# Optimization experiments

Measured on AMD Instinct MI355X. Metric: run time of the kernel, lower is better.

The kernel has to match this reference:

```python
import jax, jax.numpy as jnp
import numpy as np

# DCRNN (PEMS-BAY scale) constants
N = 325      # num_nodes
B = 64       # batch_size
T = 12       # encoder seq_len
HZ = 12      # decoder horizon
U = 64       # rnn_units
DIN = 2      # input_dim
DOUT = 1     # output_dim
K = 2        # max_diffusion_step
NM = K + 1   # num diffusion matrices (Chebyshev, single laplacian support)


def _glorot(key, shape):
    lim = float(np.sqrt(6.0 / (shape[0] + shape[1])))
    return jax.random.uniform(key, shape, jnp.float32, -lim, lim)


def setup_inputs() -> dict:
    key = jax.random.key(0)
    ks = jax.random.split(key, 8)
    # random symmetric adjacency -> scaled Laplacian support (lambda_max ~= 2 approx)
    a = np.asarray(jax.random.uniform(ks[0], (N, N)))
    a = (a + a.T) * 0.5
    a = a * (a > 0.9)
    d = a.sum(1)
    dinv = 1.0 / np.sqrt(np.maximum(d, 1e-8))
    L = np.eye(N, dtype=np.float32) - (dinv[:, None] * a * dinv[None, :]).astype(np.float32)
    support = jnp.asarray(L - np.eye(N, dtype=np.float32))  # 2L/lambda_max - I with lambda_max=2

    def cell_params(k, din):
        f = (din + U) * NM
        k1, k2 = jax.random.split(k)
        return dict(gate_W=_glorot(k1, (f, 2 * U)), gate_b=jnp.zeros((2 * U,), jnp.float32),
                    cand_W=_glorot(k2, (f, U)), cand_b=jnp.zeros((U,), jnp.float32))

    inp = {"inputs": jax.random.normal(ks[1], (T, B, N * DIN), jnp.float32),
           "support": support}
    for name, din, kk in [("enc0", DIN, ks[2]), ("enc1", U, ks[3]),
                          ("dec0", DOUT, ks[4]), ("dec1", U, ks[5])]:
        for pn, v in cell_params(kk, din).items():
            inp[f"{name}_{pn}"] = v
    inp["proj_W"] = _glorot(ks[6], (U, DOUT))
    inp["proj_b"] = jnp.zeros((DOUT,), jnp.float32)
    return inp


def _gconv(x, support, W, b):
    # x: (B, N, F). Chebyshev diffusion: x0=x, x1=Lx, x2=2Lx1-x0, ...
    xs = [x]
    x0, x1 = x, jnp.einsum('mn,bnf->bmf', support, x)
    xs.append(x1)
    for _ in range(2, K + 1):
        x2 = 2.0 * jnp.einsum('mn,bnf->bmf', support, x1) - x0
        xs.append(x2)
        x0, x1 = x1, x2
    xk = jnp.concatenate(xs, axis=-1)  # (B, N, NM*F)
    return xk @ W + b


def _gru_cell(x, h, support, gW, gb, cW, cb):
    # diffusion-conv GRU: r,u gates then candidate
    ru = jax.nn.sigmoid(_gconv(jnp.concatenate([x, h], -1), support, gW, gb))
    r, u = jnp.split(ru, 2, axis=-1)
    c = jnp.tanh(_gconv(jnp.concatenate([x, r * h], -1), support, cW, cb))
    return u * h + (1.0 - u) * c


def reference(inputs, support,
              enc0_gate_W, enc0_gate_b, enc0_cand_W, enc0_cand_b,
              enc1_gate_W, enc1_gate_b, enc1_cand_W, enc1_cand_b,
              dec0_gate_W, dec0_gate_b, dec0_cand_W, dec0_cand_b,
              dec1_gate_W, dec1_gate_b, dec1_cand_W, dec1_cand_b,
              proj_W, proj_b):
    x_seq = inputs.reshape(T, B, N, DIN)
    h0 = jnp.zeros((B, N, U), inputs.dtype)

    def enc_step(carry, x):
        h_l0, h_l1 = carry
        h_l0 = _gru_cell(x, h_l0, support, enc0_gate_W, enc0_gate_b, enc0_cand_W, enc0_cand_b)
        h_l1 = _gru_cell(h_l0, h_l1, support, enc1_gate_W, enc1_gate_b, enc1_cand_W, enc1_cand_b)
        return (h_l0, h_l1), None

    (h_l0, h_l1), _ = jax.lax.scan(enc_step, (h0, h0), x_seq)

    def dec_step(carry, _):
        d_in, hd0, hd1 = carry
        hd0 = _gru_cell(d_in, hd0, support, dec0_gate_W, dec0_gate_b, dec0_cand_W, dec0_cand_b)
        hd1 = _gru_cell(hd0, hd1, support, dec1_gate_W, dec1_gate_b, dec1_cand_W, dec1_cand_b)
        out = hd1 @ proj_W + proj_b  # (B, N, DOUT)
        return (out, hd0, hd1), out.reshape(B, N * DOUT)

    start = jnp.zeros((B, N, DOUT), inputs.dtype)  # GO symbol
    _, outputs = jax.lax.scan(dec_step, (start, h_l0, h_l1), None, length=HZ)
    return outputs  # (horizon, B, N*DOUT)
```

## Files before the change

kernel.cpp:

```cpp
#include <hip/hip_runtime.h>

constexpr int N  = 325;
constexpr int B  = 64;
constexpr int T  = 12;
constexpr int HZ = 12;
constexpr int U  = 64;
constexpr int BN = B * N;

constexpr int SSM   = 672;
constexpr int SSTIL = 42;
constexpr int SSKC  = 11;

typedef __attribute__((ext_vector_type(8))) short short8;
typedef __attribute__((ext_vector_type(4))) float floatx4;

__device__ inline unsigned short f2bf(float f) {
    unsigned u = __float_as_uint(f);
    u += 0x7fff + ((u >> 16) & 1);
    return (unsigned short)(u >> 16);
}
__device__ inline unsigned pack_hilo(float v) {
    const unsigned short hi = f2bf(v);
    const float hif = __uint_as_float(((unsigned)hi) << 16);
    const unsigned short lo = f2bf(v - hif);
    return (unsigned)hi | ((unsigned)lo << 16);
}


__global__ void zero_kernel(unsigned* __restrict__ p, long n) {
    long i = (long)blockIdx.x * blockDim.x + threadIdx.x;
    const long stride = (long)gridDim.x * blockDim.x;
    for (; i < n; i += stride) p[i] = 0u;
}

__global__ __launch_bounds__(256)
void s2_build(const float* __restrict__ S, float* __restrict__ S2)
{
    const int m = blockIdx.x;
    __shared__ float srow[N];
    for (int i = threadIdx.x; i < N; i += 256) srow[i] = S[m * N + i];
    __syncthreads();
    for (int c = threadIdx.x; c < N; c += 256) {
        float a = 0.f;
        for (int k = 0; k < N; ++k) a += srow[k] * S[k * N + c];
        S2[m * N + c] = a;
    }
}

__global__ __launch_bounds__(64)
void prepack_ss(const float* __restrict__ S, const float* __restrict__ S2,
                short* __restrict__ ssh, short* __restrict__ ssl)
{
    const int t = blockIdx.x, kc = blockIdx.y, lane = threadIdx.x;
    const int quad = lane >> 4, l15 = lane & 15;
    short8 hv, lv;
    #pragma unroll
    for (int j = 0; j < 8; ++j) {
        const int m = t * 16 + l15;
        const int k = kc * 32 + quad * 8 + j;
        float v = 0.f;
        if (k < N) {
            if (m < N) v = S[m * N + k];
            else if (m >= 336 && m < 336 + N) v = S2[(m - 336) * N + k];
        }
        const unsigned short hb = f2bf(v);
        hv[j] = (short)hb;
        lv[j] = (short)f2bf(v - __uint_as_float(((unsigned)hb) << 16));
    }
    const size_t off = ((size_t)(t * SSKC + kc) * 64 + lane);
    ((short8*)ssh)[off] = hv;
    ((short8*)ssl)[off] = lv;
}

__global__ __launch_bounds__(64)
void prepack_w(const float* __restrict__ W, short* __restrict__ Wh,
               short* __restrict__ Wl, int F, int Nout, int NT)
{
    const int kc = blockIdx.x, n = blockIdx.y, lane = threadIdx.x;
    const int quad = lane >> 4, l15 = lane & 15;
    short8 hv, lv;
    #pragma unroll
    for (int j = 0; j < 8; ++j) {
        const int k   = kc * 32 + quad * 8 + j;
        const int col = n * 16 + l15;
        const int lvl = k / F, f = k - lvl * F;
        float w = 0.f;
        if (lvl == 0)
            w = W[(size_t)f * Nout + col] - W[(size_t)(2 * F + f) * Nout + col];
        else if (lvl == 1)
            w = W[(size_t)(F + f) * Nout + col];
        else if (lvl == 2)
            w = 2.f * W[(size_t)(2 * F + f) * Nout + col];
        const unsigned short hb = f2bf(w);
        hv[j] = (short)hb;
        lv[j] = (short)f2bf(w - __uint_as_float(((unsigned)hb) << 16));
    }
    const size_t off = ((size_t)(kc * NT + n) * 64 + lane);
    ((short8*)Wh)[off] = hv;
    ((short8*)Wl)[off] = lv;
}

template<int DIN, int F, int K3P, bool RMUL>
__global__ __launch_bounds__(448, 3)
void diffuse_mfma(const short8* __restrict__ ssh, const short8* __restrict__ ssl,
                  const float* __restrict__ x, const float* __restrict__ h,
                  const float* __restrict__ ru, unsigned* __restrict__ zcat)
{
    constexpr int XST = 364;
    const int cx = blockIdx.x, b = blockIdx.y, mh = blockIdx.z;
    const int c0 = cx * 32;
    const int tid = threadIdx.x, wave = tid >> 6, lane = tid & 63;
    const int quad = lane >> 4, l15 = lane & 15;

    __shared__ unsigned xls[32 * XST];

    for (int idx = tid; idx < 352 * 32; idx += 448) {
        const int n = idx >> 5, f = idx & 31, gf = c0 + f;
        unsigned u = 0u;
        if (n < N && gf < F) {
            const int row = b * N + n;
            float v;
            if (gf < DIN) {
                v = x[(size_t)row * DIN + gf];
            } else {
                v = h[(size_t)row * U + (gf - DIN)];
                if (RMUL) v *= ru[(size_t)row * 128 + (gf - DIN)];
            }
            u = pack_hilo(v);
            if (mh == 0 && !(RMUL && gf < DIN))
                zcat[(size_t)row * K3P + gf] = u;
        }
        xls[f * XST + n] = u;
    }
    __syncthreads();

    const int tb = mh * 21 + wave * 3;

    floatx4 acc[3][2];
    #pragma unroll
    for (int i = 0; i < 3; ++i)
        #pragma unroll
        for (int n = 0; n < 2; ++n)
            acc[i][n] = (floatx4){0.f, 0.f, 0.f, 0.f};

    short8 cah[3], cal[3], nah[3], nal[3];
    #pragma unroll
    for (int i = 0; i < 3; ++i) {
        const size_t fo = (size_t)((tb + i) * SSKC) * 64 + lane;
        cah[i] = ssh[fo]; cal[i] = ssl[fo];
    }
    for (int kc = 0; kc < SSKC; ++kc) {
        if (kc + 1 < SSKC) {
            #pragma unroll
            for (int i = 0; i < 3; ++i) {
                const size_t fo = (size_t)((tb + i) * SSKC + kc + 1) * 64 + lane;
                nah[i] = ssh[fo]; nal[i] = ssl[fo];
            }
        }
        short8 bh[2], bl[2];
        const int koff = kc * 32 + quad * 8;
        #pragma unroll
        for (int n = 0; n < 2; ++n) {
            const uint4 u0 = *(const uint4*)&xls[(n * 16 + l15) * XST + koff];
            const uint4 u1 = *(const uint4*)&xls[(n * 16 + l15) * XST + koff + 4];
            const unsigned uu[8] = {u0.x, u0.y, u0.z, u0.w, u1.x, u1.y, u1.z, u1.w};
            #pragma unroll
            for (int j = 0; j < 8; ++j) {
                bh[n][j] = (short)(uu[j] & 0xffffu);
                bl[n][j] = (short)(uu[j] >> 16);
            }
        }
        #pragma unroll
        for (int i = 0; i < 3; ++i)
            #pragma unroll
            for (int n = 0; n < 2; ++n) {
                acc[i][n] = __builtin_amdgcn_mfma_f32_16x16x32_bf16(cah[i], bh[n], acc[i][n], 0, 0, 0);
                acc[i][n] = __builtin_amdgcn_mfma_f32_16x16x32_bf16(cah[i], bl[n], acc[i][n], 0, 0, 0);
                acc[i][n] = __builtin_amdgcn_mfma_f32_16x16x32_bf16(cal[i], bh[n], acc[i][n], 0, 0, 0);
            }
        if (kc + 1 < SSKC) {
            #pragma unroll
            for (int i = 0; i < 3; ++i) { cah[i] = nah[i]; cal[i] = nal[i]; }
        }
    }

    #pragma unroll
    for (int i = 0; i < 3; ++i) {
        const int t = tb + i;
        #pragma unroll
        for (int n = 0; n < 2; ++n) {
            const int col = c0 + n * 16 + l15;
            if (col >= F) continue;
            #pragma unroll
            for (int r = 0; r < 4; ++r) {
                const int m = t * 16 + quad * 4 + r;
                if (m < N)
                    zcat[(size_t)(b * N + m) * K3P + F + col] = pack_hilo(acc[i][n][r]);
                else if (m >= 336 && m < 336 + N)
                    zcat[(size_t)(b * N + (m - 336)) * K3P + 2 * F + col] = pack_hilo(acc[i][n][r]);
            }
        }
    }
}

__global__ __launch_bounds__(256)
void dense_gate_mfma(const unsigned* __restrict__ zcat, int K3p,
                     const short8* __restrict__ Wh, const short8* __restrict__ Wl,
                     const float* __restrict__ bias, float* __restrict__ ru)
{
    constexpr int NT = 4;
    const int tid = threadIdx.x, wave = tid >> 6, lane = tid & 63;
    const int quad = lane >> 4, l15 = lane & 15;
    const int row0 = blockIdx.x * 64 + wave * 16;
    const int nb = blockIdx.y * NT;

    floatx4 acc[NT];
    #pragma unroll
    for (int n = 0; n < NT; ++n) {
        const float bv = bias[(nb + n) * 16 + l15];
        acc[n] = (floatx4){bv, bv, bv, bv};
    }
    const unsigned* __restrict__ zrow = zcat + (size_t)(row0 + l15) * K3p + quad * 8;
    const int KC = K3p >> 5;
    for (int kc = 0; kc < KC; ++kc) {
        const uint4* p = (const uint4*)(zrow + kc * 32);
        const uint4 u0 = p[0], u1 = p[1];
        const unsigned uu[8] = {u0.x, u0.y, u0.z, u0.w, u1.x, u1.y, u1.z, u1.w};
        short8 ahi, alo;
        #pragma unroll
        for (int j = 0; j < 8; ++j) {
            ahi[j] = (short)(uu[j] & 0xffffu);
            alo[j] = (short)(uu[j] >> 16);
        }
        const short8* __restrict__ wh = Wh + (size_t)(kc * 8 + nb) * 64 + lane;
        const short8* __restrict__ wl = Wl + (size_t)(kc * 8 + nb) * 64 + lane;
        #pragma unroll
        for (int n = 0; n < NT; ++n) {
            const short8 bh = wh[n * 64], bl = wl[n * 64];
            acc[n] = __builtin_amdgcn_mfma_f32_16x16x32_bf16(ahi, bh, acc[n], 0, 0, 0);
            acc[n] = __builtin_amdgcn_mfma_f32_16x16x32_bf16(ahi, bl, acc[n], 0, 0, 0);
            acc[n] = __builtin_amdgcn_mfma_f32_16x16x32_bf16(alo, bh, acc[n], 0, 0, 0);
        }
    }
    #pragma unroll
    for (int n = 0; n < NT; ++n) {
        const int col = (nb + n) * 16 + l15;
        #pragma unroll
        for (int r = 0; r < 4; ++r) {
            const int row = row0 + quad * 4 + r;
            ru[(size_t)row * 128 + col] = 1.f / (1.f + __expf(-acc[n][r]));
        }
    }
}

template<bool PROJ>
__global__ __launch_bounds__(256)
void dense_cand_mfma(const unsigned* __restrict__ zcat, int K3p,
                     const short8* __restrict__ Wh, const short8* __restrict__ Wl,
                     const float* __restrict__ bias, const float* __restrict__ ru,
                     float* __restrict__ h, const float* __restrict__ pW,
                     const float* __restrict__ pb, float* __restrict__ outp,
                     float* __restrict__ dec_in)
{
    constexpr int NT = PROJ ? 4 : 2;
    const int tid = threadIdx.x, wave = tid >> 6, lane = tid & 63;
    const int quad = lane >> 4, l15 = lane & 15;
    const int row0 = blockIdx.x * 64 + wave * 16;
    const int nb = PROJ ? 0 : blockIdx.y * NT;

    floatx4 acc[NT];
    #pragma unroll
    for (int n = 0; n < NT; ++n) {
        const float bv = bias[(nb + n) * 16 + l15];
        acc[n] = (floatx4){bv, bv, bv, bv};
    }
    const unsigned* __restrict__ zrow = zcat + (size_t)(row0 + l15) * K3p + quad * 8;
    const int KC = K3p >> 5;
    for (int kc = 0; kc < KC; ++kc) {
        const uint4* p = (const uint4*)(zrow + kc * 32);
        const uint4 u0 = p[0], u1 = p[1];
        const unsigned uu[8] = {u0.x, u0.y, u0.z, u0.w, u1.x, u1.y, u1.z, u1.w};
        short8 ahi, alo;
        #pragma unroll
        for (int j = 0; j < 8; ++j) {
            ahi[j] = (short)(uu[j] & 0xffffu);
            alo[j] = (short)(uu[j] >> 16);
        }
        const short8* __restrict__ wh = Wh + (size_t)(kc * 4 + nb) * 64 + lane;
        const short8* __restrict__ wl = Wl + (size_t)(kc * 4 + nb) * 64 + lane;
        #pragma unroll
        for (int n = 0; n < NT; ++n) {
            const short8 bh = wh[n * 64], bl = wl[n * 64];
            acc[n] = __builtin_amdgcn_mfma_f32_16x16x32_bf16(ahi, bh, acc[n], 0, 0, 0);
            acc[n] = __builtin_amdgcn_mfma_f32_16x16x32_bf16(ahi, bl, acc[n], 0, 0, 0);
            acc[n] = __builtin_amdgcn_mfma_f32_16x16x32_bf16(alo, bh, acc[n], 0, 0, 0);
        }
    }
    float pr[4] = {0.f, 0.f, 0.f, 0.f};
    #pragma unroll
    for (int n = 0; n < NT; ++n) {
        const int col = (nb + n) * 16 + l15;
        float pw = 0.f;
        if constexpr (PROJ) pw = pW[col];
        #pragma unroll
        for (int r = 0; r < 4; ++r) {
            const int row = row0 + quad * 4 + r;
            const float c  = tanhf(acc[n][r]);
            const float ug = ru[(size_t)row * 128 + 64 + col];
            const float hv = h[(size_t)row * 64 + col];
            const float hn = ug * hv + (1.f - ug) * c;
            h[(size_t)row * 64 + col] = hn;
            if constexpr (PROJ) pr[r] += hn * pw;
        }
    }
    if constexpr (PROJ) {
        #pragma unroll
        for (int r = 0; r < 4; ++r) {
            float v = pr[r];
            v += __shfl_xor(v, 1); v += __shfl_xor(v, 2);
            v += __shfl_xor(v, 4); v += __shfl_xor(v, 8);
            if (l15 == 0) {
                const int row = row0 + quad * 4 + r;
                const float o = v + pb[0];
                outp[row]   = o;
                dec_in[row] = o;
            }
        }
    }
}


extern "C" void kernel_launch(void* const* d_in, const int* in_sizes, int n_in,
                              void* d_out, int out_size, void* d_ws, size_t ws_size,
                              hipStream_t stream)
{
    const float* inputs = (const float*)d_in[0];
    const float* S      = (const float*)d_in[1];
    const float* Wt[4][4];
    for (int l = 0; l < 4; ++l)
        for (int j = 0; j < 4; ++j)
            Wt[l][j] = (const float*)d_in[2 + l * 4 + j];
    const float* pW = (const float*)d_in[18];
    const float* pb = (const float*)d_in[19];
    float* out = (float*)d_out;

    float*    ws     = (float*)d_ws;
    float*    h0     = ws;
    float*    h1     = h0 + (size_t)BN * U;
    float*    dec_in = h1 + (size_t)BN * U;
    float*    ru     = dec_in + BN;
    unsigned* zcat   = (unsigned*)(ru + (size_t)BN * 128);
    float*    S2     = (float*)(zcat + (size_t)BN * 384);
    char*     pp     = (char*)(S2 + (size_t)N * N);
    pp = (char*)(((uintptr_t)pp + 15) & ~(uintptr_t)15);

    short* ssh = (short*)pp;
    short* ssl = ssh + (size_t)SSTIL * SSKC * 64 * 8;
    char*  wpbase = (char*)(ssl + (size_t)SSTIL * SSKC * 64 * 8);

    const int Fs[4]   = {66, 128, 65, 128};
    const int K3ps[4] = {224, 384, 224, 384};
    short *Wgh[4], *Wgl[4], *Wch[4], *Wcl[4];
    size_t off = 0;
    for (int l = 0; l < 4; ++l) {
        const size_t ge = (size_t)K3ps[l] * 128, ce = (size_t)K3ps[l] * 64;
        Wgh[l] = (short*)(wpbase + off); off += ge * 2;
        Wgl[l] = (short*)(wpbase + off); off += ge * 2;
        Wch[l] = (short*)(wpbase + off); off += ce * 2;
        Wcl[l] = (short*)(wpbase + off); off += ce * 2;
    }

    const long zn = (long)BN * (U + U + 128) + BN + (long)BN * 384;
    zero_kernel<<<2048, 256, 0, stream>>>((unsigned*)h0, zn);

    s2_build<<<N, 256, 0, stream>>>(S, S2);
    prepack_ss<<<dim3(SSTIL, SSKC), 64, 0, stream>>>(S, S2, ssh, ssl);
    for (int l = 0; l < 4; ++l) {
        prepack_w<<<dim3(K3ps[l] / 32, 8), 64, 0, stream>>>(Wt[l][0], Wgh[l], Wgl[l],
                                                            Fs[l], 128, 8);
        prepack_w<<<dim3(K3ps[l] / 32, 4), 64, 0, stream>>>(Wt[l][2], Wch[l], Wcl[l],
                                                            Fs[l], 64, 4);
    }

    const short8* SSH = (const short8*)ssh;
    const short8* SSL = (const short8*)ssl;

    for (int t = 0; t < T; ++t) {
        const float* x = inputs + (size_t)t * BN * 2;
        diffuse_mfma<2, 66, 224, false><<<dim3(3, B, 2), 448, 0, stream>>>(SSH, SSL, x, h0, ru, zcat);
        dense_gate_mfma<<<dim3(BN / 64, 2), 256, 0, stream>>>(zcat, 224, (short8*)Wgh[0], (short8*)Wgl[0], Wt[0][1], ru);
        diffuse_mfma<2, 66, 224, true><<<dim3(3, B, 2), 448, 0, stream>>>(SSH, SSL, x, h0, ru, zcat);
        dense_cand_mfma<false><<<dim3(BN / 64, 2), 256, 0, stream>>>(zcat, 224, (short8*)Wch[0], (short8*)Wcl[0],
                                                                     Wt[0][3], ru, h0, nullptr, nullptr, nullptr, nullptr);
        diffuse_mfma<64, 128, 384, false><<<dim3(4, B, 2), 448, 0, stream>>>(SSH, SSL, h0, h1, ru, zcat);
        dense_gate_mfma<<<dim3(BN / 64, 2), 256, 0, stream>>>(zcat, 384, (short8*)Wgh[1], (short8*)Wgl[1], Wt[1][1], ru);
        diffuse_mfma<64, 128, 384, true><<<dim3(4, B, 2), 448, 0, stream>>>(SSH, SSL, h0, h1, ru, zcat);
        dense_cand_mfma<false><<<dim3(BN / 64, 2), 256, 0, stream>>>(zcat, 384, (short8*)Wch[1], (short8*)Wcl[1],
                                                                     Wt[1][3], ru, h1, nullptr, nullptr, nullptr, nullptr);
    }
    for (int hz = 0; hz < HZ; ++hz) {
        diffuse_mfma<1, 65, 224, false><<<dim3(3, B, 2), 448, 0, stream>>>(SSH, SSL, dec_in, h0, ru, zcat);
        dense_gate_mfma<<<dim3(BN / 64, 2), 256, 0, stream>>>(zcat, 224, (short8*)Wgh[2], (short8*)Wgl[2], Wt[2][1], ru);
        diffuse_mfma<1, 65, 224, true><<<dim3(3, B, 2), 448, 0, stream>>>(SSH, SSL, dec_in, h0, ru, zcat);
        dense_cand_mfma<false><<<dim3(BN / 64, 2), 256, 0, stream>>>(zcat, 224, (short8*)Wch[2], (short8*)Wcl[2],
                                                                     Wt[2][3], ru, h0, nullptr, nullptr, nullptr, nullptr);
        diffuse_mfma<64, 128, 384, false><<<dim3(4, B, 2), 448, 0, stream>>>(SSH, SSL, h0, h1, ru, zcat);
        dense_gate_mfma<<<dim3(BN / 64, 2), 256, 0, stream>>>(zcat, 384, (short8*)Wgh[3], (short8*)Wgl[3], Wt[3][1], ru);
        diffuse_mfma<64, 128, 384, true><<<dim3(4, B, 2), 448, 0, stream>>>(SSH, SSL, h0, h1, ru, zcat);
        dense_cand_mfma<true><<<BN / 64, 256, 0, stream>>>(zcat, 384, (short8*)Wch[3], (short8*)Wcl[3],
                                                           Wt[3][3], ru, h1, pW, pb,
                                                           out + (size_t)hz * BN, dec_in);
    }
}
```

Before: 4.518 ms.

## Pipeline encoder layers across timesteps and skip redundant input diffusion

The encoder is skewed so that layer 0 at step s and layer 1 at step s-1 run in the same launches. Merged diffuse, gate and candidate kernels pick a layer from blockIdx.z, and each layer gets its own ru and zcat buffers. This halves the number of encoder kernel launches and puts more blocks in each grid to fill the GPU. Separately, the reset-multiplied diffusion pass for the 64-wide input layers now starts at column block 2, so the input-feature columns computed in the first pass are not diffused again. The cost is a larger workspace and extra branching inside the merged kernels.

```diff
diff --git a/kernel.cpp b/kernel.cpp
--- a/kernel.cpp
+++ b/kernel.cpp
@@ -7,9 +7,9 @@
 constexpr int U  = 64;
 constexpr int BN = B * N;
 
-constexpr int SSM   = 672;
 constexpr int SSTIL = 42;
 constexpr int SSKC  = 11;
+constexpr int XST   = 364;
 
 typedef __attribute__((ext_vector_type(8))) short short8;
 typedef __attribute__((ext_vector_type(4))) float floatx4;
@@ -24,6 +24,15 @@
     const float hif = __uint_as_float(((unsigned)hi) << 16);
     const unsigned short lo = f2bf(v - hif);
     return (unsigned)hi | ((unsigned)lo << 16);
+}
+__device__ inline void unpack8(const uint4 u0, const uint4 u1,
+                               short8& h, short8& l) {
+    const unsigned uu[8] = {u0.x, u0.y, u0.z, u0.w, u1.x, u1.y, u1.z, u1.w};
+    #pragma unroll
+    for (int j = 0; j < 8; ++j) {
+        h[j] = (short)(uu[j] & 0xffffu);
+        l[j] = (short)(uu[j] >> 16);
+    }
 }
 
 
@@ -101,18 +110,15 @@
 }
 
 template<int DIN, int F, int K3P, bool RMUL>
-__global__ __launch_bounds__(448, 3)
-void diffuse_mfma(const short8* __restrict__ ssh, const short8* __restrict__ ssl,
-                  const float* __restrict__ x, const float* __restrict__ h,
-                  const float* __restrict__ ru, unsigned* __restrict__ zcat)
-{
-    constexpr int XST = 364;
-    const int cx = blockIdx.x, b = blockIdx.y, mh = blockIdx.z;
+__device__ __forceinline__ void diffuse_body(
+    const short8* __restrict__ ssh, const short8* __restrict__ ssl,
+    const float* __restrict__ x, const float* __restrict__ h,
+    const float* __restrict__ ru, unsigned* __restrict__ zcat,
+    int cx, int b, int mh, unsigned* __restrict__ xls)
+{
     const int c0 = cx * 32;
     const int tid = threadIdx.x, wave = tid >> 6, lane = tid & 63;
     const int quad = lane >> 4, l15 = lane & 15;
-
-    __shared__ unsigned xls[32 * XST];
 
     for (int idx = tid; idx < 352 * 32; idx += 448) {
         const int n = idx >> 5, f = idx & 31, gf = c0 + f;
@@ -163,12 +169,7 @@
         for (int n = 0; n < 2; ++n) {
             const uint4 u0 = *(const uint4*)&xls[(n * 16 + l15) * XST + koff];
             const uint4 u1 = *(const uint4*)&xls[(n * 16 + l15) * XST + koff + 4];
-            const unsigned uu[8] = {u0.x, u0.y, u0.z, u0.w, u1.x, u1.y, u1.z, u1.w};
-            #pragma unroll
-            for (int j = 0; j < 8; ++j) {
-                bh[n][j] = (short)(uu[j] & 0xffffu);
-                bl[n][j] = (short)(uu[j] >> 16);
-            }
+            unpack8(u0, u1, bh[n], bl[n]);
         }
         #pragma unroll
         for (int i = 0; i < 3; ++i)
@@ -203,16 +204,15 @@
     }
 }
 
-__global__ __launch_bounds__(256)
-void dense_gate_mfma(const unsigned* __restrict__ zcat, int K3p,
-                     const short8* __restrict__ Wh, const short8* __restrict__ Wl,
-                     const float* __restrict__ bias, float* __restrict__ ru)
+
+__device__ __forceinline__ void gate_body(const unsigned* __restrict__ zcat,
+    int K3p, const short8* __restrict__ Wh, const short8* __restrict__ Wl,
+    const float* __restrict__ bias, float* __restrict__ ru, int bx, int nb)
 {
     constexpr int NT = 4;
     const int tid = threadIdx.x, wave = tid >> 6, lane = tid & 63;
     const int quad = lane >> 4, l15 = lane & 15;
-    const int row0 = blockIdx.x * 64 + wave * 16;
-    const int nb = blockIdx.y * NT;
+    const int row0 = bx * 64 + wave * 16;
 
     floatx4 acc[NT];
     #pragma unroll
@@ -224,14 +224,8 @@
     const int KC = K3p >> 5;
     for (int kc = 0; kc < KC; ++kc) {
         const uint4* p = (const uint4*)(zrow + kc * 32);
-        const uint4 u0 = p[0], u1 = p[1];
-        const unsigned uu[8] = {u0.x, u0.y, u0.z, u0.w, u1.x, u1.y, u1.z, u1.w};
         short8 ahi, alo;
-        #pragma unroll
-        for (int j = 0; j < 8; ++j) {
-            ahi[j] = (short)(uu[j] & 0xffffu);
-            alo[j] = (short)(uu[j] >> 16);
-        }
+        unpack8(p[0], p[1], ahi, alo);
         const short8* __restrict__ wh = Wh + (size_t)(kc * 8 + nb) * 64 + lane;
         const short8* __restrict__ wl = Wl + (size_t)(kc * 8 + nb) * 64 + lane;
         #pragma unroll
@@ -253,20 +247,15 @@
     }
 }
 
-template<bool PROJ>
-__global__ __launch_bounds__(256)
-void dense_cand_mfma(const unsigned* __restrict__ zcat, int K3p,
-                     const short8* __restrict__ Wh, const short8* __restrict__ Wl,
-                     const float* __restrict__ bias, const float* __restrict__ ru,
-                     float* __restrict__ h, const float* __restrict__ pW,
-                     const float* __restrict__ pb, float* __restrict__ outp,
-                     float* __restrict__ dec_in)
-{
-    constexpr int NT = PROJ ? 4 : 2;
+__device__ __forceinline__ void cand_body(const unsigned* __restrict__ zcat,
+    int K3p, const short8* __restrict__ Wh, const short8* __restrict__ Wl,
+    const float* __restrict__ bias, const float* __restrict__ ru,
+    float* __restrict__ h, int bx, int nb)
+{
+    constexpr int NT = 2;
     const int tid = threadIdx.x, wave = tid >> 6, lane = tid & 63;
     const int quad = lane >> 4, l15 = lane & 15;
-    const int row0 = blockIdx.x * 64 + wave * 16;
-    const int nb = PROJ ? 0 : blockIdx.y * NT;
+    const int row0 = bx * 64 + wave * 16;
 
     floatx4 acc[NT];
     #pragma unroll
@@ -278,14 +267,8 @@
     const int KC = K3p >> 5;
     for (int kc = 0; kc < KC; ++kc) {
         const uint4* p = (const uint4*)(zrow + kc * 32);
-        const uint4 u0 = p[0], u1 = p[1];
-        const unsigned uu[8] = {u0.x, u0.y, u0.z, u0.w, u1.x, u1.y, u1.z, u1.w};
         short8 ahi, alo;
-        #pragma unroll
-        for (int j = 0; j < 8; ++j) {
-            ahi[j] = (short)(uu[j] & 0xffffu);
-            alo[j] = (short)(uu[j] >> 16);
-        }
+        unpack8(p[0], p[1], ahi, alo);
         const short8* __restrict__ wh = Wh + (size_t)(kc * 4 + nb) * 64 + lane;
         const short8* __restrict__ wl = Wl + (size_t)(kc * 4 + nb) * 64 + lane;
         #pragma unroll
@@ -296,12 +279,89 @@
             acc[n] = __builtin_amdgcn_mfma_f32_16x16x32_bf16(alo, bh, acc[n], 0, 0, 0);
         }
     }
-    float pr[4] = {0.f, 0.f, 0.f, 0.f};
     #pragma unroll
     for (int n = 0; n < NT; ++n) {
         const int col = (nb + n) * 16 + l15;
-        float pw = 0.f;
-        if constexpr (PROJ) pw = pW[col];
+        #pragma unroll
+        for (int r = 0; r < 4; ++r) {
+            const int row = row0 + quad * 4 + r;
+            const float c  = tanhf(acc[n][r]);
+            const float ug = ru[(size_t)row * 128 + 64 + col];
+            const float hv = h[(size_t)row * 64 + col];
+            h[(size_t)row * 64 + col] = ug * hv + (1.f - ug) * c;
+        }
+    }
+}
+
+
+template<int DIN, int F, int K3P, bool RMUL, int CB>
+__global__ __launch_bounds__(448, 3)
+void diffuse_solo(const short8* __restrict__ ssh, const short8* __restrict__ ssl,
+                  const float* __restrict__ x, const float* __restrict__ h,
+                  const float* __restrict__ ru, unsigned* __restrict__ zcat)
+{
+    __shared__ __align__(16) unsigned xls[32 * XST];
+    diffuse_body<DIN, F, K3P, RMUL>(ssh, ssl, x, h, ru, zcat,
+                                    CB + blockIdx.x, blockIdx.y, blockIdx.z, xls);
+}
+
+__global__ __launch_bounds__(256)
+void gate_solo(const unsigned* __restrict__ zcat, int K3p,
+               const short8* __restrict__ Wh, const short8* __restrict__ Wl,
+               const float* __restrict__ bias, float* __restrict__ ru)
+{
+    gate_body(zcat, K3p, Wh, Wl, bias, ru, blockIdx.x, blockIdx.y * 4);
+}
+
+__global__ __launch_bounds__(256)
+void cand_solo(const unsigned* __restrict__ zcat, int K3p,
+               const short8* __restrict__ Wh, const short8* __restrict__ Wl,
+               const float* __restrict__ bias, const float* __restrict__ ru,
+               float* __restrict__ h)
+{
+    cand_body(zcat, K3p, Wh, Wl, bias, ru, h, blockIdx.x, blockIdx.y * 2);
+}
+
+__global__ __launch_bounds__(256)
+void cand_proj(const unsigned* __restrict__ zcat, int K3p,
+               const short8* __restrict__ Wh, const short8* __restrict__ Wl,
+               const float* __restrict__ bias, const float* __restrict__ ru,
+               float* __restrict__ h, const float* __restrict__ pW,
+               const float* __restrict__ pb, float* __restrict__ outp,
+               float* __restrict__ dec_in)
+{
+    constexpr int NT = 4;
+    const int tid = threadIdx.x, wave = tid >> 6, lane = tid & 63;
+    const int quad = lane >> 4, l15 = lane & 15;
+    const int row0 = blockIdx.x * 64 + wave * 16;
+
+    floatx4 acc[NT];
+    #pragma unroll
+    for (int n = 0; n < NT; ++n) {
+        const float bv = bias[n * 16 + l15];
+        acc[n] = (floatx4){bv, bv, bv, bv};
+    }
+    const unsigned* __restrict__ zrow = zcat + (size_t)(row0 + l15) * K3p + quad * 8;
+    const int KC = K3p >> 5;
+    for (int kc = 0; kc < KC; ++kc) {
+        const uint4* p = (const uint4*)(zrow + kc * 32);
+        short8 ahi, alo;
+        unpack8(p[0], p[1], ahi, alo);
+        const short8* __restrict__ wh = Wh + (size_t)(kc * 4) * 64 + lane;
+        const short8* __restrict__ wl = Wl + (size_t)(kc * 4) * 64 + lane;
+        #pragma unroll
+        for (int n = 0; n < NT; ++n) {
+            const short8 bh = wh[n * 64], bl = wl[n * 64];
+            acc[n] = __builtin_amdgcn_mfma_f32_16x16x32_bf16(ahi, bh, acc[n], 0, 0, 0);
+            acc[n] = __builtin_amdgcn_mfma_f32_16x16x32_bf16(ahi, bl, acc[n], 0, 0, 0);
+            acc[n] = __builtin_amdgcn_mfma_f32_16x16x32_bf16(alo, bh, acc[n], 0, 0, 0);
+        }
+    }
+    float pr[4] = {0.f, 0.f, 0.f, 0.f};
+    #pragma unroll
+    for (int n = 0; n < NT; ++n) {
+        const int col = n * 16 + l15;
+        const float pw = pW[col];
         #pragma unroll
         for (int r = 0; r < 4; ++r) {
             const int row = row0 + quad * 4 + r;
@@ -310,23 +370,76 @@
             const float hv = h[(size_t)row * 64 + col];
             const float hn = ug * hv + (1.f - ug) * c;
             h[(size_t)row * 64 + col] = hn;
-            if constexpr (PROJ) pr[r] += hn * pw;
-        }
-    }
-    if constexpr (PROJ) {
-        #pragma unroll
-        for (int r = 0; r < 4; ++r) {
-            float v = pr[r];
-            v += __shfl_xor(v, 1); v += __shfl_xor(v, 2);
-            v += __shfl_xor(v, 4); v += __shfl_xor(v, 8);
-            if (l15 == 0) {
-                const int row = row0 + quad * 4 + r;
-                const float o = v + pb[0];
-                outp[row]   = o;
-                dec_in[row] = o;
-            }
-        }
-    }
+            pr[r] += hn * pw;
+        }
+    }
+    #pragma unroll
+    for (int r = 0; r < 4; ++r) {
+        float v = pr[r];
+        v += __shfl_xor(v, 1); v += __shfl_xor(v, 2);
+        v += __shfl_xor(v, 4); v += __shfl_xor(v, 8);
+        if (l15 == 0) {
+            const int row = row0 + quad * 4 + r;
+            const float o = v + pb[0];
+            outp[row]   = o;
+            dec_in[row] = o;
+        }
+    }
+}
+
+
+struct DuoDP {
+    const short8 *ssh, *ssl;
+    const float *xA, *hA, *ruA; unsigned* zA;
+    const float *xB, *hB, *ruB; unsigned* zB;
+    int cbB;
+};
+
+template<bool RM>
+__global__ __launch_bounds__(448, 3)
+void diffuse_duo(DuoDP P)
+{
+    __shared__ __align__(16) unsigned xls[32 * XST];
+    const int zz = blockIdx.z;
+    if (zz < 2) {
+        if ((int)blockIdx.x < 3)
+            diffuse_body<2, 66, 224, RM>(P.ssh, P.ssl, P.xA, P.hA, P.ruA, P.zA,
+                                         blockIdx.x, blockIdx.y, zz, xls);
+    } else {
+        if ((int)blockIdx.x < 4 - P.cbB)
+            diffuse_body<64, 128, 384, RM>(P.ssh, P.ssl, P.xB, P.hB, P.ruB, P.zB,
+                                           P.cbB + blockIdx.x, blockIdx.y, zz - 2, xls);
+    }
+}
+
+struct DuoGP {
+    const unsigned* zA; const short8 *WhA, *WlA; const float* bA; float* ruA;
+    const unsigned* zB; const short8 *WhB, *WlB; const float* bB; float* ruB;
+};
+
+__global__ __launch_bounds__(256)
+void gate_duo(DuoGP P)
+{
+    if (blockIdx.z == 0)
+        gate_body(P.zA, 224, P.WhA, P.WlA, P.bA, P.ruA, blockIdx.x, blockIdx.y * 4);
+    else
+        gate_body(P.zB, 384, P.WhB, P.WlB, P.bB, P.ruB, blockIdx.x, blockIdx.y * 4);
+}
+
+struct DuoCP {
+    const unsigned* zA; const short8 *WhA, *WlA; const float* bA;
+    const float* ruA; float* hA;
+    const unsigned* zB; const short8 *WhB, *WlB; const float* bB;
+    const float* ruB; float* hB;
+};
+
+__global__ __launch_bounds__(256)
+void cand_duo(DuoCP P)
+{
+    if (blockIdx.z == 0)
+        cand_body(P.zA, 224, P.WhA, P.WlA, P.bA, P.ruA, P.hA, blockIdx.x, blockIdx.y * 2);
+    else
+        cand_body(P.zB, 384, P.WhB, P.WlB, P.bB, P.ruB, P.hB, blockIdx.x, blockIdx.y * 2);
 }
 
 
@@ -348,9 +461,11 @@
     float*    h0     = ws;
     float*    h1     = h0 + (size_t)BN * U;
     float*    dec_in = h1 + (size_t)BN * U;
-    float*    ru     = dec_in + BN;
-    unsigned* zcat   = (unsigned*)(ru + (size_t)BN * 128);
-    float*    S2     = (float*)(zcat + (size_t)BN * 384);
+    float*    ruA    = dec_in + BN;
+    float*    ruB    = ruA + (size_t)BN * 128;
+    unsigned* zcatA  = (unsigned*)(ruB + (size_t)BN * 128);
+    unsigned* zcatB  = zcatA + (size_t)BN * 224;
+    float*    S2     = (float*)(zcatB + (size_t)BN * 384);
     char*     pp     = (char*)(S2 + (size_t)N * N);
     pp = (char*)(((uintptr_t)pp + 15) & ~(uintptr_t)15);
 
@@ -370,7 +485,7 @@
         Wcl[l] = (short*)(wpbase + off); off += ce * 2;
     }
 
-    const long zn = (long)BN * (U + U + 128) + BN + (long)BN * 384;
+    const long zn = (long)BN * (2 * U) + BN + (long)BN * 256 + (long)BN * (224 + 384);
     zero_kernel<<<2048, 256, 0, stream>>>((unsigned*)h0, zn);
 
     s2_build<<<N, 256, 0, stream>>>(S, S2);
@@ -385,30 +500,58 @@
     const short8* SSH = (const short8*)ssh;
     const short8* SSL = (const short8*)ssl;
 
-    for (int t = 0; t < T; ++t) {
-        const float* x = inputs + (size_t)t * BN * 2;
-        diffuse_mfma<2, 66, 224, false><<<dim3(3, B, 2), 448, 0, stream>>>(SSH, SSL, x, h0, ru, zcat);
-        dense_gate_mfma<<<dim3(BN / 64, 2), 256, 0, stream>>>(zcat, 224, (short8*)Wgh[0], (short8*)Wgl[0], Wt[0][1], ru);
-        diffuse_mfma<2, 66, 224, true><<<dim3(3, B, 2), 448, 0, stream>>>(SSH, SSL, x, h0, ru, zcat);
-        dense_cand_mfma<false><<<dim3(BN / 64, 2), 256, 0, stream>>>(zcat, 224, (short8*)Wch[0], (short8*)Wcl[0],
-                                                                     Wt[0][3], ru, h0, nullptr, nullptr, nullptr, nullptr);
-        diffuse_mfma<64, 128, 384, false><<<dim3(4, B, 2), 448, 0, stream>>>(SSH, SSL, h0, h1, ru, zcat);
-        dense_gate_mfma<<<dim3(BN / 64, 2), 256, 0, stream>>>(zcat, 384, (short8*)Wgh[1], (short8*)Wgl[1], Wt[1][1], ru);
-        diffuse_mfma<64, 128, 384, true><<<dim3(4, B, 2), 448, 0, stream>>>(SSH, SSL, h0, h1, ru, zcat);
-        dense_cand_mfma<false><<<dim3(BN / 64, 2), 256, 0, stream>>>(zcat, 384, (short8*)Wch[1], (short8*)Wcl[1],
-                                                                     Wt[1][3], ru, h1, nullptr, nullptr, nullptr, nullptr);
-    }
+    for (int s = 0; s <= T; ++s) {
+        const float* x0 = inputs + (size_t)s * BN * 2;
+        const bool a = (s < T), b1 = (s >= 1);
+        if (a && b1) {
+            DuoDP dp{SSH, SSL, x0, h0, nullptr, zcatA, h0, h1, nullptr, zcatB, 0};
+            diffuse_duo<false><<<dim3(4, B, 4), 448, 0, stream>>>(dp);
+            DuoGP gp{zcatA, (short8*)Wgh[0], (short8*)Wgl[0], Wt[0][1], ruA,
+                     zcatB, (short8*)Wgh[1], (short8*)Wgl[1], Wt[1][1], ruB};
+            gate_duo<<<dim3(BN / 64, 2, 2), 256, 0, stream>>>(gp);
+            DuoDP dp2{SSH, SSL, x0, h0, ruA, zcatA, h0, h1, ruB, zcatB, 2};
+            diffuse_duo<true><<<dim3(3, B, 4), 448, 0, stream>>>(dp2);
+            DuoCP cp{zcatA, (short8*)Wch[0], (short8*)Wcl[0], Wt[0][3], ruA, h0,
+                     zcatB, (short8*)Wch[1], (short8*)Wcl[1], Wt[1][3], ruB, h1};
+            cand_duo<<<dim3(BN / 64, 2, 2), 256, 0, stream>>>(cp);
+        } else if (a) {
+            diffuse_solo<2, 66, 224, false, 0><<<dim3(3, B, 2), 448, 0, stream>>>(
+                SSH, SSL, x0, h0, nullptr, zcatA);
+            gate_solo<<<dim3(BN / 64, 2), 256, 0, stream>>>(
+                zcatA, 224, (short8*)Wgh[0], (short8*)Wgl[0], Wt[0][1], ruA);
+            diffuse_solo<2, 66, 224, true, 0><<<dim3(3, B, 2), 448, 0, stream>>>(
+                SSH, SSL, x0, h0, ruA, zcatA);
+            cand_solo<<<dim3(BN / 64, 2), 256, 0, stream>>>(
+                zcatA, 224, (short8*)Wch[0], (short8*)Wcl[0], Wt[0][3], ruA, h0);
+        } else {
+            diffuse_solo<64, 128, 384, false, 0><<<dim3(4, B, 2), 448, 0, stream>>>(
+                SSH, SSL, h0, h1, nullptr, zcatB);
+            gate_solo<<<dim3(BN / 64, 2), 256, 0, stream>>>(
+                zcatB, 384, (short8*)Wgh[1], (short8*)Wgl[1], Wt[1][1], ruB);
+            diffuse_solo<64, 128, 384, true, 2><<<dim3(2, B, 2), 448, 0, stream>>>(
+                SSH, SSL, h0, h1, ruB, zcatB);
+            cand_solo<<<dim3(BN / 64, 2), 256, 0, stream>>>(
+                zcatB, 384, (short8*)Wch[1], (short8*)Wcl[1], Wt[1][3], ruB, h1);
+        }
+    }
+
     for (int hz = 0; hz < HZ; ++hz) {
-        diffuse_mfma<1, 65, 224, false><<<dim3(3, B, 2), 448, 0, stream>>>(SSH, SSL, dec_in, h0, ru, zcat);
-        dense_gate_mfma<<<dim3(BN / 64, 2), 256, 0, stream>>>(zcat, 224, (short8*)Wgh[2], (short8*)Wgl[2], Wt[2][1], ru);
-        diffuse_mfma<1, 65, 224, true><<<dim3(3, B, 2), 448, 0, stream>>>(SSH, SSL, dec_in, h0, ru, zcat);
-        dense_cand_mfma<false><<<dim3(BN / 64, 2), 256, 0, stream>>>(zcat, 224, (short8*)Wch[2], (short8*)Wcl[2],
-                                                                     Wt[2][3], ru, h0, nullptr, nullptr, nullptr, nullptr);
-        diffuse_mfma<64, 128, 384, false><<<dim3(4, B, 2), 448, 0, stream>>>(SSH, SSL, h0, h1, ru, zcat);
-        dense_gate_mfma<<<dim3(BN / 64, 2), 256, 0, stream>>>(zcat, 384, (short8*)Wgh[3], (short8*)Wgl[3], Wt[3][1], ru);
-        diffuse_mfma<64, 128, 384, true><<<dim3(4, B, 2), 448, 0, stream>>>(SSH, SSL, h0, h1, ru, zcat);
-        dense_cand_mfma<true><<<BN / 64, 256, 0, stream>>>(zcat, 384, (short8*)Wch[3], (short8*)Wcl[3],
-                                                           Wt[3][3], ru, h1, pW, pb,
-                                                           out + (size_t)hz * BN, dec_in);
-    }
-}
+        diffuse_solo<1, 65, 224, false, 0><<<dim3(3, B, 2), 448, 0, stream>>>(
+            SSH, SSL, dec_in, h0, nullptr, zcatB);
+        gate_solo<<<dim3(BN / 64, 2), 256, 0, stream>>>(
+            zcatB, 224, (short8*)Wgh[2], (short8*)Wgl[2], Wt[2][1], ruA);
+        diffuse_solo<1, 65, 224, true, 0><<<dim3(3, B, 2), 448, 0, stream>>>(
+            SSH, SSL, dec_in, h0, ruA, zcatB);
+        cand_solo<<<dim3(BN / 64, 2), 256, 0, stream>>>(
+            zcatB, 224, (short8*)Wch[2], (short8*)Wcl[2], Wt[2][3], ruA, h0);
+        diffuse_solo<64, 128, 384, false, 0><<<dim3(4, B, 2), 448, 0, stream>>>(
+            SSH, SSL, h0, h1, nullptr, zcatB);
+        gate_solo<<<dim3(BN / 64, 2), 256, 0, stream>>>(
+            zcatB, 384, (short8*)Wgh[3], (short8*)Wgl[3], Wt[3][1], ruA);
+        diffuse_solo<64, 128, 384, true, 2><<<dim3(2, B, 2), 448, 0, stream>>>(
+            SSH, SSL, h0, h1, ruA, zcatB);
+        cand_proj<<<BN / 64, 256, 0, stream>>>(
+            zcatB, 384, (short8*)Wch[3], (short8*)Wcl[3], Wt[3][3], ruA, h1,
+            pW, pb, out + (size_t)hz * BN, dec_in);
+    }
+}
```

Result: faster. 4.082 ms (-9.6%).
